# Performance work log

Hardware: AMD Instinct MI355X
Metric: run time of the kernel (lower is better)

Reference implementation:

```python
import jax, jax.numpy as jnp
import numpy as np

B, T, D, H = 2, 2048, 1024, 16
HD = D // H  # head_dim = 64

def setup_inputs() -> dict:
    key = jax.random.key(0)
    ks = jax.random.split(key, 5)
    s = 0.02
    return {
        "x": jax.random.normal(ks[0], (B, T, D), dtype=jnp.float32),
        "w_qkv": jax.random.normal(ks[1], (3 * D, D), dtype=jnp.float32) * s,
        "b_qkv": jax.random.normal(ks[2], (3 * D,), dtype=jnp.float32) * s,
        "w_proj": jax.random.normal(ks[3], (D, D), dtype=jnp.float32) * s,
        "b_proj": jax.random.normal(ks[4], (D,), dtype=jnp.float32) * s,
    }

def reference(x, w_qkv, b_qkv, w_proj, b_proj):
    b, t, c = x.shape
    h, hd = H, HD
    scale = hd ** -0.5
    # qkv projection (torch Linear: x @ W^T + b)
    qkv = x @ w_qkv.T + b_qkv                      # [b, t, 3c]
    q, k, v = jnp.split(qkv, 3, axis=-1)
    # b t (h d) -> b h t d
    reshape = lambda z: z.reshape(b, t, h, hd).transpose(0, 2, 1, 3)
    q, k, v = reshape(q), reshape(k), reshape(v)
    scores = jnp.einsum("bhqd,bhkd->bhqk", q, k) * scale  # [b, h, t, t]
    causal = jnp.triu(jnp.ones((t, t), dtype=bool), k=1)   # True above diag
    scores = jnp.where(causal[None, None], -jnp.inf, scores)
    attn = jax.nn.softmax(scores, axis=-1)
    out = jnp.einsum("bhqk,bhkd->bhqd", attn, v)            # [b, h, t, d]
    out = out.transpose(0, 2, 1, 3).reshape(b, t, c)        # b h t d -> b t (h d)
    return out @ w_proj.T + b_proj
```

## Files before the change

kernel.cpp:

```cpp
#include <hip/hip_runtime.h>
#include <hip/hip_bf16.h>

#define Bq 2
#define Tq 2048
#define Dq 1024
#define Hq 16
#define HDq 64

typedef __attribute__((ext_vector_type(8))) short short8;
typedef __attribute__((ext_vector_type(4))) float f32x4;

__device__ __forceinline__ unsigned short f2bf(float f) {
  union { float f; unsigned int i; } v; v.f = f;
  unsigned int r = v.i + 0x7fffu + ((v.i >> 16) & 1u);
  return (unsigned short)(r >> 16);
}
__device__ __forceinline__ unsigned short f2bf_fast(float f) {
  union { float f; unsigned int i; } v; v.f = f;
  return (unsigned short)((v.i + 0x8000u) >> 16);
}

__device__ __forceinline__ short8 cvt8(const float* __restrict__ g) {
  const float4* gp = (const float4*)g;
  float4 x0 = gp[0], x1 = gp[1];
  short8 v;
  v[0] = (short)f2bf(x0.x); v[1] = (short)f2bf(x0.y);
  v[2] = (short)f2bf(x0.z); v[3] = (short)f2bf(x0.w);
  v[4] = (short)f2bf(x1.x); v[5] = (short)f2bf(x1.y);
  v[6] = (short)f2bf(x1.z); v[7] = (short)f2bf(x1.w);
  return v;
}

__device__ __forceinline__ void async_cp16(const void* g, void* l) {
  __builtin_amdgcn_global_load_lds(
      (const __attribute__((address_space(1))) void*)g,
      (__attribute__((address_space(3))) void*)l, 16, 0, 0);
}

constexpr int NXC = (Bq * Tq * Dq) / 8;
constexpr int NW1C = (3 * Dq * Dq) / 8;
constexpr int NW2C = (Dq * Dq) / 8;

__global__ __launch_bounds__(256)
void cvt_all(const float* __restrict__ x, const float* __restrict__ w1,
             const float* __restrict__ w2, unsigned short* __restrict__ xo,
             unsigned short* __restrict__ w1o, unsigned short* __restrict__ w2o)
{
  int i = blockIdx.x * 256 + threadIdx.x;
  const float* src; unsigned short* dst; int j;
  if (i < NXC)              { src = x;  dst = xo;  j = i; }
  else if (i < NXC + NW1C)  { src = w1; dst = w1o; j = i - NXC; }
  else                      { src = w2; dst = w2o; j = i - NXC - NW1C; }
  *(short8*)&dst[(size_t)j * 8] = cvt8(src + (size_t)j * 8);
}

template<int EPI, int BM_, int BN_>
__global__ __launch_bounds__(256)
void gemm_bt(const unsigned short* __restrict__ Ab, const unsigned short* __restrict__ Wb,
             const float* __restrict__ bias, float* __restrict__ outp,
             int K, int N,
             unsigned short* __restrict__ qo, unsigned short* __restrict__ ko,
             unsigned short* __restrict__ vo)
{
  constexpr int WM = BM_ / 2, WN = BN_ / 2;
  constexpr int NI = WM / 16;
  constexpr int NJ = WN / 16;
  constexpr int NAI = BM_ / 32;
  constexpr int NBI = BN_ / 32;
  __shared__ unsigned short As[2 * BM_ * 32];
  __shared__ unsigned short Bs[2 * BN_ * 32];

  const int t = threadIdx.x;
  const int lane = t & 63, w = t >> 6;
  const int m0 = blockIdx.y * BM_, n0 = blockIdx.x * BN_;
  const int fr = lane & 15, qd = lane >> 4;
  const int wm = (w >> 1) * WM, wn = (w & 1) * WN;

  f32x4 acc[NI][NJ] = {};

  for (int k0 = 0; k0 < K; k0 += 64) {
    __syncthreads();
    #pragma unroll
    for (int j = 0; j < NAI; j++) {
      int G = j * 256 + t;
      int panel = G / (BM_ * 4), rowg = (G / 4) % BM_, colg = G & 3;
      async_cp16(Ab + (size_t)(m0 + rowg) * K + k0 + panel * 32 + colg * 8, &As[G * 8]);
    }
    #pragma unroll
    for (int j = 0; j < NBI; j++) {
      int G = j * 256 + t;
      int panel = G / (BN_ * 4), rowg = (G / 4) % BN_, colg = G & 3;
      async_cp16(Wb + (size_t)(n0 + rowg) * K + k0 + panel * 32 + colg * 8, &Bs[G * 8]);
    }
    __syncthreads();
    #pragma unroll
    for (int kh = 0; kh < 2; kh++) {
      short8 af[NI], bf[NJ];
      #pragma unroll
      for (int ib = 0; ib < NI; ib++)
        af[ib] = *(const short8*)&As[kh * (BM_ * 32) + (wm + ib * 16 + fr) * 32 + qd * 8];
      #pragma unroll
      for (int jb = 0; jb < NJ; jb++)
        bf[jb] = *(const short8*)&Bs[kh * (BN_ * 32) + (wn + jb * 16 + fr) * 32 + qd * 8];
      #pragma unroll
      for (int ib = 0; ib < NI; ib++)
        #pragma unroll
        for (int jb = 0; jb < NJ; jb++)
          acc[ib][jb] = __builtin_amdgcn_mfma_f32_16x16x32_bf16(af[ib], bf[jb], acc[ib][jb], 0, 0, 0);
    }
  }

  #pragma unroll
  for (int jb = 0; jb < NJ; jb++) {
    int col = n0 + wn + jb * 16 + fr;
    float bv = bias[col];
    if (EPI == 0) {
      int which = col >> 10;
      int rem = col & 1023;
      int hh = rem >> 6, dd = rem & 63;
      #pragma unroll
      for (int ib = 0; ib < NI; ib++) {
        int row4 = m0 + wm + ib * 16 + qd * 4;
        int bb = row4 >> 11, tt = row4 & (Tq - 1);
        if (which == 2) {
          unsigned lo = (unsigned)f2bf(acc[ib][jb][0] + bv)
                      | ((unsigned)f2bf(acc[ib][jb][1] + bv) << 16);
          unsigned hi = (unsigned)f2bf(acc[ib][jb][2] + bv)
                      | ((unsigned)f2bf(acc[ib][jb][3] + bv) << 16);
          uint2 pk; pk.x = lo; pk.y = hi;
          *(uint2*)&vo[((size_t)(bb * Hq + hh) * HDq + dd) * Tq + tt] = pk;
        } else {
          unsigned short* dst = (which == 0) ? qo : ko;
          #pragma unroll
          for (int r = 0; r < 4; r++)
            dst[((size_t)(bb * Hq + hh) * Tq + tt + r) * HDq + dd] = f2bf(acc[ib][jb][r] + bv);
        }
      }
    } else {
      #pragma unroll
      for (int ib = 0; ib < NI; ib++)
        #pragma unroll
        for (int r = 0; r < 4; r++) {
          int row = m0 + wm + ib * 16 + qd * 4 + r;
          outp[(size_t)row * N + col] = acc[ib][jb][r] + bv;
        }
    }
  }
}

constexpr int AP = 72;

template<bool DIAG>
__device__ __forceinline__ void strip_one(
    const short8 aq0, const short8 aq1,
    const short8 (&bk)[4][2], const short8 (&bv)[4][2], const short8 ones,
    unsigned short* __restrict__ PsRow, int fr, int qd, int qbase,
    f32x4 (&oacc)[4], f32x4& lacc, float SCL)
{
  f32x4 s4[4] = {};
  #pragma unroll
  for (int nb = 0; nb < 4; nb++) {
    s4[nb] = __builtin_amdgcn_mfma_f32_16x16x32_bf16(aq0, bk[nb][0], s4[nb], 0, 0, 0);
    s4[nb] = __builtin_amdgcn_mfma_f32_16x16x32_bf16(aq1, bk[nb][1], s4[nb], 0, 0, 0);
  }
  #pragma unroll
  for (int nb = 0; nb < 4; nb++)
    #pragma unroll
    for (int reg = 0; reg < 4; reg++) {
      float pv = exp2f(s4[nb][reg] * SCL);
      if (DIAG && (nb * 16 + fr) > (qbase + reg)) pv = 0.f;
      PsRow[(qd * 4 + reg) * AP + nb * 16 + fr] = f2bf_fast(pv);
    }
  short8 ap0 = *(const short8*)&PsRow[fr * AP + qd * 8];
  short8 ap1 = *(const short8*)&PsRow[fr * AP + 32 + qd * 8];
  lacc = __builtin_amdgcn_mfma_f32_16x16x32_bf16(ap0, ones, lacc, 0, 0, 0);
  lacc = __builtin_amdgcn_mfma_f32_16x16x32_bf16(ap1, ones, lacc, 0, 0, 0);
  #pragma unroll
  for (int db = 0; db < 4; db++) {
    oacc[db] = __builtin_amdgcn_mfma_f32_16x16x32_bf16(ap0, bv[db][0], oacc[db], 0, 0, 0);
    oacc[db] = __builtin_amdgcn_mfma_f32_16x16x32_bf16(ap1, bv[db][1], oacc[db], 0, 0, 0);
  }
}

template<bool SMALLDIAG>
__device__ __forceinline__ void strip_dual(
    const short8 (&aqB)[2], const short8 (&aqA)[2],
    const short8 (&bk)[4][2], const short8 (&bv)[4][2], const short8 ones,
    unsigned short* __restrict__ PsB, unsigned short* __restrict__ PsA,
    int fr, int qd, int qbase,
    f32x4 (&oB)[4], f32x4& lB, f32x4 (&oA)[4], f32x4& lA, float SCL)
{
  f32x4 sB[4] = {}, sA[4] = {};
  #pragma unroll
  for (int nb = 0; nb < 4; nb++) {
    sB[nb] = __builtin_amdgcn_mfma_f32_16x16x32_bf16(aqB[0], bk[nb][0], sB[nb], 0, 0, 0);
    sA[nb] = __builtin_amdgcn_mfma_f32_16x16x32_bf16(aqA[0], bk[nb][0], sA[nb], 0, 0, 0);
  }
  #pragma unroll
  for (int nb = 0; nb < 4; nb++) {
    sB[nb] = __builtin_amdgcn_mfma_f32_16x16x32_bf16(aqB[1], bk[nb][1], sB[nb], 0, 0, 0);
    sA[nb] = __builtin_amdgcn_mfma_f32_16x16x32_bf16(aqA[1], bk[nb][1], sA[nb], 0, 0, 0);
  }
  #pragma unroll
  for (int nb = 0; nb < 4; nb++)
    #pragma unroll
    for (int reg = 0; reg < 4; reg++) {
      float pvB = exp2f(sB[nb][reg] * SCL);
      float pvA = exp2f(sA[nb][reg] * SCL);
      if (SMALLDIAG && (nb * 16 + fr) > (qbase + reg)) pvA = 0.f;
      PsB[(qd * 4 + reg) * AP + nb * 16 + fr] = f2bf_fast(pvB);
      PsA[(qd * 4 + reg) * AP + nb * 16 + fr] = f2bf_fast(pvA);
    }
  short8 apB0 = *(const short8*)&PsB[fr * AP + qd * 8];
  short8 apB1 = *(const short8*)&PsB[fr * AP + 32 + qd * 8];
  short8 apA0 = *(const short8*)&PsA[fr * AP + qd * 8];
  short8 apA1 = *(const short8*)&PsA[fr * AP + 32 + qd * 8];
  lB = __builtin_amdgcn_mfma_f32_16x16x32_bf16(apB0, ones, lB, 0, 0, 0);
  lA = __builtin_amdgcn_mfma_f32_16x16x32_bf16(apA0, ones, lA, 0, 0, 0);
  lB = __builtin_amdgcn_mfma_f32_16x16x32_bf16(apB1, ones, lB, 0, 0, 0);
  lA = __builtin_amdgcn_mfma_f32_16x16x32_bf16(apA1, ones, lA, 0, 0, 0);
  #pragma unroll
  for (int db = 0; db < 4; db++) {
    oB[db] = __builtin_amdgcn_mfma_f32_16x16x32_bf16(apB0, bv[db][0], oB[db], 0, 0, 0);
    oA[db] = __builtin_amdgcn_mfma_f32_16x16x32_bf16(apA0, bv[db][0], oA[db], 0, 0, 0);
  }
  #pragma unroll
  for (int db = 0; db < 4; db++) {
    oB[db] = __builtin_amdgcn_mfma_f32_16x16x32_bf16(apB1, bv[db][1], oB[db], 0, 0, 0);
    oA[db] = __builtin_amdgcn_mfma_f32_16x16x32_bf16(apA1, bv[db][1], oA[db], 0, 0, 0);
  }
}

__global__ __launch_bounds__(256, 2)
void attn_fwd(const unsigned short* __restrict__ qb, const unsigned short* __restrict__ kb,
              const unsigned short* __restrict__ vtb, unsigned short* __restrict__ ab)
{
  __shared__ unsigned short Ks[2][64 * 64];
  __shared__ unsigned short Vts[2][64 * 64];
  __shared__ unsigned short Ps[128 * AP];

  const int t = threadIdx.x, w = t >> 6, lane = t & 63;
  const int fr = lane & 15, qd = lane >> 4;
  const int p = blockIdx.x;
  const int bh = blockIdx.y;
  const int sB = 31 - p;
  const int sA = p;
  const int s0t[2] = { sB * 64, sA * 64 };
  const int ktB = sB;
  const int qbase = w * 16 + qd * 4;

  short8 aq[2][2];
  #pragma unroll
  for (int tl = 0; tl < 2; tl++) {
    const unsigned short* Qg = qb + ((size_t)bh * Tq + s0t[tl]) * HDq;
    #pragma unroll
    for (int c = 0; c < 2; c++)
      aq[tl][c] = *(const short8*)(Qg + (w * 16 + fr) * 64 + c * 32 + qd * 8);
  }

  const unsigned short* Kbh = kb + (size_t)bh * Tq * HDq;
  const unsigned short* Vbh = vtb + (size_t)bh * HDq * Tq;

  const int off0 = ((qd ^ (fr & 7)) * 8);
  const int off1 = off0 ^ 32;

  const int G0 = 2 * w * 64 + lane, G1 = G0 + 64;
  const int r0 = G0 >> 3, g0 = (G0 & 7) ^ (r0 & 7);
  const int r1 = G1 >> 3, g1 = (G1 & 7) ^ (r1 & 7);

  short8 ones;
  #pragma unroll
  for (int j = 0; j < 8; j++) ones[j] = (short)0x3F80;

  f32x4 oacc[2][4] = {};
  f32x4 lacc[2] = {};
  const float SCL = 0.125f * 1.44269504088896f;

  unsigned short* PsB = &Ps[(0 * 64 + w * 16) * AP];
  unsigned short* PsA = &Ps[(1 * 64 + w * 16) * AP];

  async_cp16(Kbh + (size_t)r0 * 64 + g0 * 8, &Ks[0][G0 * 8]);
  async_cp16(Vbh + (size_t)r0 * Tq + g0 * 8, &Vts[0][G0 * 8]);
  async_cp16(Kbh + (size_t)r1 * 64 + g1 * 8, &Ks[0][G1 * 8]);
  async_cp16(Vbh + (size_t)r1 * Tq + g1 * 8, &Vts[0][G1 * 8]);

  for (int kt = 0; kt <= ktB; kt++) {
    const int cur = kt & 1;
    __syncthreads();
    if (kt < ktB) {
      const int nxt = cur ^ 1;
      const size_t kofs = (size_t)(kt + 1) * 64;
      async_cp16(Kbh + (kofs + r0) * 64 + g0 * 8, &Ks[nxt][G0 * 8]);
      async_cp16(Vbh + (size_t)r0 * Tq + kofs + g0 * 8, &Vts[nxt][G0 * 8]);
      async_cp16(Kbh + (kofs + r1) * 64 + g1 * 8, &Ks[nxt][G1 * 8]);
      async_cp16(Vbh + (size_t)r1 * Tq + kofs + g1 * 8, &Vts[nxt][G1 * 8]);
    }

    short8 bk[4][2], bv[4][2];
    #pragma unroll
    for (int nb = 0; nb < 4; nb++) {
      bk[nb][0] = *(const short8*)&Ks[cur][(nb * 16 + fr) * 64 + off0];
      bk[nb][1] = *(const short8*)&Ks[cur][(nb * 16 + fr) * 64 + off1];
      bv[nb][0] = *(const short8*)&Vts[cur][(nb * 16 + fr) * 64 + off0];
      bv[nb][1] = *(const short8*)&Vts[cur][(nb * 16 + fr) * 64 + off1];
    }

    if (kt < sA) {
      strip_dual<false>(aq[0], aq[1], bk, bv, ones, PsB, PsA, fr, qd, qbase,
                        oacc[0], lacc[0], oacc[1], lacc[1], SCL);
    } else if (kt == sA) {
      strip_dual<true >(aq[0], aq[1], bk, bv, ones, PsB, PsA, fr, qd, qbase,
                        oacc[0], lacc[0], oacc[1], lacc[1], SCL);
    } else if (kt == ktB) {
      strip_one<true >(aq[0][0], aq[0][1], bk, bv, ones, PsB, fr, qd, qbase,
                       oacc[0], lacc[0], SCL);
    } else {
      strip_one<false>(aq[0][0], aq[0][1], bk, bv, ones, PsB, fr, qd, qbase,
                       oacc[0], lacc[0], SCL);
    }
  }

  #pragma unroll
  for (int tl = 0; tl < 2; tl++)
    #pragma unroll
    for (int reg = 0; reg < 4; reg++) {
      float linv = 1.0f / lacc[tl][reg];
      size_t rowoff = ((size_t)(bh >> 4) * Tq + s0t[tl] + w * 16 + qd * 4 + reg) * Dq
                    + (bh & 15) * HDq;
      #pragma unroll
      for (int db = 0; db < 4; db++)
        ab[rowoff + db * 16 + fr] = f2bf(oacc[tl][db][reg] * linv);
    }
}

extern "C" void kernel_launch(void* const* d_in, const int* in_sizes, int n_in,
                              void* d_out, int out_size, void* d_ws, size_t ws_size,
                              hipStream_t stream) {
  const float* x      = (const float*)d_in[0];
  const float* w_qkv  = (const float*)d_in[1];
  const float* b_qkv  = (const float*)d_in[2];
  const float* w_proj = (const float*)d_in[3];
  const float* b_proj = (const float*)d_in[4];
  float* out = (float*)d_out;

  unsigned short* ws = (unsigned short*)d_ws;
  const size_t NE = (size_t)Bq * Hq * Tq * HDq;
  unsigned short* qb  = ws;
  unsigned short* kb  = ws + NE;
  unsigned short* vtb = ws + 2 * NE;
  unsigned short* ab  = ws + 3 * NE;
  unsigned short* xb  = ws + 4 * NE;
  unsigned short* wqb = xb + (size_t)NXC * 8;
  unsigned short* wpb = wqb + (size_t)NW1C * 8;

  dim3 blk(256);
  cvt_all<<<dim3((NXC + NW1C + NW2C) >> 8), blk, 0, stream>>>(x, w_qkv, w_proj, xb, wqb, wpb);

  dim3 g1(3 * Dq / 128, Bq * Tq / 128);
  gemm_bt<0, 128, 128><<<g1, blk, 0, stream>>>(xb, wqb, b_qkv, nullptr,
                                               Dq, 3 * Dq, qb, kb, vtb);
  dim3 g2(16, Bq * Hq);
  attn_fwd<<<g2, blk, 0, stream>>>(qb, kb, vtb, ab);
  dim3 g3(Dq / 128, Bq * Tq / 64);
  gemm_bt<1, 64, 128><<<g3, blk, 0, stream>>>(ab, wpb, b_proj, out,
                                              Dq, Dq, nullptr, nullptr, nullptr);
}
```

Baseline: 190.9 us.

## Compute transposed scores in attention, reshuffle P in registers, drop LDS P buffer

The attention kernel now computes S^T (K as the A operand), so each lane holds probabilities along the key dimension. It packs them with v_cvt_pk_bf16_f32 and rearranges them with permlane swaps into the PV operand layout, which removes the LDS round trip for P. The softmax scale times log2(e) is folded into Q in the QKV GEMM epilogue. The paired causal-balancing tiles are replaced by one q-tile per block with 4 blocks/SM occupancy and setprio around the MFMA bursts. The cost is losing the load-balanced strip pairing, plus gfx950-specific permlane instructions and a different rounding of P.

```diff
diff --git a/kernel.cpp b/kernel.cpp
--- a/kernel.cpp
+++ b/kernel.cpp
@@ -14,10 +14,6 @@
   union { float f; unsigned int i; } v; v.f = f;
   unsigned int r = v.i + 0x7fffu + ((v.i >> 16) & 1u);
   return (unsigned short)(r >> 16);
-}
-__device__ __forceinline__ unsigned short f2bf_fast(float f) {
-  union { float f; unsigned int i; } v; v.f = f;
-  return (unsigned short)((v.i + 0x8000u) >> 16);
 }
 
 __device__ __forceinline__ short8 cvt8(const float* __restrict__ g) {
@@ -37,9 +33,16 @@
       (__attribute__((address_space(3))) void*)l, 16, 0, 0);
 }
 
+__device__ __forceinline__ void permswap(unsigned &a, unsigned &b) {
+  asm("v_permlane32_swap_b32 %0, %1" : "+v"(a), "+v"(b));
+  asm("v_permlane16_swap_b32 %0, %1" : "+v"(a), "+v"(b));
+}
+
 constexpr int NXC = (Bq * Tq * Dq) / 8;
 constexpr int NW1C = (3 * Dq * Dq) / 8;
 constexpr int NW2C = (Dq * Dq) / 8;
+
+#define QSCL 0.18033688011112042f
 
 __global__ __launch_bounds__(256)
 void cvt_all(const float* __restrict__ x, const float* __restrict__ w1,
@@ -131,9 +134,11 @@
           *(uint2*)&vo[((size_t)(bb * Hq + hh) * HDq + dd) * Tq + tt] = pk;
         } else {
           unsigned short* dst = (which == 0) ? qo : ko;
+          float scl = (which == 0) ? QSCL : 1.0f;
           #pragma unroll
           for (int r = 0; r < 4; r++)
-            dst[((size_t)(bb * Hq + hh) * Tq + tt + r) * HDq + dd] = f2bf(acc[ib][jb][r] + bv);
+            dst[((size_t)(bb * Hq + hh) * Tq + tt + r) * HDq + dd] =
+                f2bf((acc[ib][jb][r] + bv) * scl);
         }
       }
     } else {
@@ -148,31 +153,62 @@
   }
 }
 
-constexpr int AP = 72;
 
 template<bool DIAG>
-__device__ __forceinline__ void strip_one(
-    const short8 aq0, const short8 aq1,
-    const short8 (&bk)[4][2], const short8 (&bv)[4][2], const short8 ones,
-    unsigned short* __restrict__ PsRow, int fr, int qd, int qbase,
-    f32x4 (&oacc)[4], f32x4& lacc, float SCL)
+__device__ __forceinline__ void strip_iter(
+    const unsigned short* __restrict__ Ksb, const unsigned short* __restrict__ Vtsb,
+    const short8 (&aq)[2], const short8 ones,
+    int fr, int qd, int off0, int off1, int thr,
+    f32x4 (&oacc)[4], f32x4& lacc)
 {
+  short8 bk[4][2];
+  #pragma unroll
+  for (int nb = 0; nb < 4; nb++) {
+    bk[nb][0] = *(const short8*)&Ksb[(nb * 16 + fr) * 64 + off0];
+    bk[nb][1] = *(const short8*)&Ksb[(nb * 16 + fr) * 64 + off1];
+  }
   f32x4 s4[4] = {};
+  __builtin_amdgcn_s_setprio(1);
+  #pragma unroll
+  for (int nb = 0; nb < 4; nb++)
+    s4[nb] = __builtin_amdgcn_mfma_f32_16x16x32_bf16(bk[nb][0], aq[0], s4[nb], 0, 0, 0);
+  #pragma unroll
+  for (int nb = 0; nb < 4; nb++)
+    s4[nb] = __builtin_amdgcn_mfma_f32_16x16x32_bf16(bk[nb][1], aq[1], s4[nb], 0, 0, 0);
+  __builtin_amdgcn_s_setprio(0);
+
+  unsigned x[4][2];
   #pragma unroll
   for (int nb = 0; nb < 4; nb++) {
-    s4[nb] = __builtin_amdgcn_mfma_f32_16x16x32_bf16(aq0, bk[nb][0], s4[nb], 0, 0, 0);
-    s4[nb] = __builtin_amdgcn_mfma_f32_16x16x32_bf16(aq1, bk[nb][1], s4[nb], 0, 0, 0);
-  }
-  #pragma unroll
-  for (int nb = 0; nb < 4; nb++)
+    float p[4];
     #pragma unroll
     for (int reg = 0; reg < 4; reg++) {
-      float pv = exp2f(s4[nb][reg] * SCL);
-      if (DIAG && (nb * 16 + fr) > (qbase + reg)) pv = 0.f;
-      PsRow[(qd * 4 + reg) * AP + nb * 16 + fr] = f2bf_fast(pv);
-    }
-  short8 ap0 = *(const short8*)&PsRow[fr * AP + qd * 8];
-  short8 ap1 = *(const short8*)&PsRow[fr * AP + 32 + qd * 8];
+      p[reg] = exp2f(s4[nb][reg]);
+      if (DIAG && (nb * 16 + qd * 4 + reg) > thr) p[reg] = 0.f;
+    }
+    asm("v_cvt_pk_bf16_f32 %0, %1, %2" : "=v"(x[nb][0]) : "v"(p[0]), "v"(p[1]));
+    asm("v_cvt_pk_bf16_f32 %0, %1, %2" : "=v"(x[nb][1]) : "v"(p[2]), "v"(p[3]));
+  }
+  permswap(x[0][0], x[1][0]);
+  permswap(x[0][1], x[1][1]);
+  permswap(x[2][0], x[3][0]);
+  permswap(x[2][1], x[3][1]);
+
+  short8 ap0, ap1;
+  {
+    union { unsigned u[4]; short8 s; } c0, c1;
+    c0.u[0] = x[0][0]; c0.u[1] = x[0][1]; c0.u[2] = x[1][0]; c0.u[3] = x[1][1];
+    c1.u[0] = x[2][0]; c1.u[1] = x[2][1]; c1.u[2] = x[3][0]; c1.u[3] = x[3][1];
+    ap0 = c0.s; ap1 = c1.s;
+  }
+
+  short8 bv[4][2];
+  #pragma unroll
+  for (int db = 0; db < 4; db++) {
+    bv[db][0] = *(const short8*)&Vtsb[(db * 16 + fr) * 64 + off0];
+    bv[db][1] = *(const short8*)&Vtsb[(db * 16 + fr) * 64 + off1];
+  }
+  __builtin_amdgcn_s_setprio(1);
   lacc = __builtin_amdgcn_mfma_f32_16x16x32_bf16(ap0, ones, lacc, 0, 0, 0);
   lacc = __builtin_amdgcn_mfma_f32_16x16x32_bf16(ap1, ones, lacc, 0, 0, 0);
   #pragma unroll
@@ -180,83 +216,28 @@
     oacc[db] = __builtin_amdgcn_mfma_f32_16x16x32_bf16(ap0, bv[db][0], oacc[db], 0, 0, 0);
     oacc[db] = __builtin_amdgcn_mfma_f32_16x16x32_bf16(ap1, bv[db][1], oacc[db], 0, 0, 0);
   }
-}
-
-template<bool SMALLDIAG>
-__device__ __forceinline__ void strip_dual(
-    const short8 (&aqB)[2], const short8 (&aqA)[2],
-    const short8 (&bk)[4][2], const short8 (&bv)[4][2], const short8 ones,
-    unsigned short* __restrict__ PsB, unsigned short* __restrict__ PsA,
-    int fr, int qd, int qbase,
-    f32x4 (&oB)[4], f32x4& lB, f32x4 (&oA)[4], f32x4& lA, float SCL)
-{
-  f32x4 sB[4] = {}, sA[4] = {};
-  #pragma unroll
-  for (int nb = 0; nb < 4; nb++) {
-    sB[nb] = __builtin_amdgcn_mfma_f32_16x16x32_bf16(aqB[0], bk[nb][0], sB[nb], 0, 0, 0);
-    sA[nb] = __builtin_amdgcn_mfma_f32_16x16x32_bf16(aqA[0], bk[nb][0], sA[nb], 0, 0, 0);
-  }
-  #pragma unroll
-  for (int nb = 0; nb < 4; nb++) {
-    sB[nb] = __builtin_amdgcn_mfma_f32_16x16x32_bf16(aqB[1], bk[nb][1], sB[nb], 0, 0, 0);
-    sA[nb] = __builtin_amdgcn_mfma_f32_16x16x32_bf16(aqA[1], bk[nb][1], sA[nb], 0, 0, 0);
-  }
-  #pragma unroll
-  for (int nb = 0; nb < 4; nb++)
-    #pragma unroll
-    for (int reg = 0; reg < 4; reg++) {
-      float pvB = exp2f(sB[nb][reg] * SCL);
-      float pvA = exp2f(sA[nb][reg] * SCL);
-      if (SMALLDIAG && (nb * 16 + fr) > (qbase + reg)) pvA = 0.f;
-      PsB[(qd * 4 + reg) * AP + nb * 16 + fr] = f2bf_fast(pvB);
-      PsA[(qd * 4 + reg) * AP + nb * 16 + fr] = f2bf_fast(pvA);
-    }
-  short8 apB0 = *(const short8*)&PsB[fr * AP + qd * 8];
-  short8 apB1 = *(const short8*)&PsB[fr * AP + 32 + qd * 8];
-  short8 apA0 = *(const short8*)&PsA[fr * AP + qd * 8];
-  short8 apA1 = *(const short8*)&PsA[fr * AP + 32 + qd * 8];
-  lB = __builtin_amdgcn_mfma_f32_16x16x32_bf16(apB0, ones, lB, 0, 0, 0);
-  lA = __builtin_amdgcn_mfma_f32_16x16x32_bf16(apA0, ones, lA, 0, 0, 0);
-  lB = __builtin_amdgcn_mfma_f32_16x16x32_bf16(apB1, ones, lB, 0, 0, 0);
-  lA = __builtin_amdgcn_mfma_f32_16x16x32_bf16(apA1, ones, lA, 0, 0, 0);
-  #pragma unroll
-  for (int db = 0; db < 4; db++) {
-    oB[db] = __builtin_amdgcn_mfma_f32_16x16x32_bf16(apB0, bv[db][0], oB[db], 0, 0, 0);
-    oA[db] = __builtin_amdgcn_mfma_f32_16x16x32_bf16(apA0, bv[db][0], oA[db], 0, 0, 0);
-  }
-  #pragma unroll
-  for (int db = 0; db < 4; db++) {
-    oB[db] = __builtin_amdgcn_mfma_f32_16x16x32_bf16(apB1, bv[db][1], oB[db], 0, 0, 0);
-    oA[db] = __builtin_amdgcn_mfma_f32_16x16x32_bf16(apA1, bv[db][1], oA[db], 0, 0, 0);
-  }
-}
-
-__global__ __launch_bounds__(256, 2)
+  __builtin_amdgcn_s_setprio(0);
+}
+
+__global__ __launch_bounds__(256, 4)
 void attn_fwd(const unsigned short* __restrict__ qb, const unsigned short* __restrict__ kb,
               const unsigned short* __restrict__ vtb, unsigned short* __restrict__ ab)
 {
   __shared__ unsigned short Ks[2][64 * 64];
   __shared__ unsigned short Vts[2][64 * 64];
-  __shared__ unsigned short Ps[128 * AP];
 
   const int t = threadIdx.x, w = t >> 6, lane = t & 63;
   const int fr = lane & 15, qd = lane >> 4;
-  const int p = blockIdx.x;
-  const int bh = blockIdx.y;
-  const int sB = 31 - p;
-  const int sA = p;
-  const int s0t[2] = { sB * 64, sA * 64 };
-  const int ktB = sB;
-  const int qbase = w * 16 + qd * 4;
-
-  short8 aq[2][2];
-  #pragma unroll
-  for (int tl = 0; tl < 2; tl++) {
-    const unsigned short* Qg = qb + ((size_t)bh * Tq + s0t[tl]) * HDq;
-    #pragma unroll
-    for (int c = 0; c < 2; c++)
-      aq[tl][c] = *(const short8*)(Qg + (w * 16 + fr) * 64 + c * 32 + qd * 8);
-  }
+  const int bh = blockIdx.x;
+  const int s = 31 - (int)blockIdx.y;
+  const int s0 = s * 64;
+  const int thr = w * 16 + fr;
+
+  short8 aq[2];
+  const unsigned short* Qg = qb + ((size_t)bh * Tq + s0) * HDq;
+  #pragma unroll
+  for (int c = 0; c < 2; c++)
+    aq[c] = *(const short8*)(Qg + (w * 16 + fr) * 64 + c * 32 + qd * 8);
 
   const unsigned short* Kbh = kb + (size_t)bh * Tq * HDq;
   const unsigned short* Vbh = vtb + (size_t)bh * HDq * Tq;
@@ -272,65 +253,36 @@
   #pragma unroll
   for (int j = 0; j < 8; j++) ones[j] = (short)0x3F80;
 
-  f32x4 oacc[2][4] = {};
-  f32x4 lacc[2] = {};
-  const float SCL = 0.125f * 1.44269504088896f;
-
-  unsigned short* PsB = &Ps[(0 * 64 + w * 16) * AP];
-  unsigned short* PsA = &Ps[(1 * 64 + w * 16) * AP];
+  f32x4 oacc[4] = {};
+  f32x4 lacc = {};
 
   async_cp16(Kbh + (size_t)r0 * 64 + g0 * 8, &Ks[0][G0 * 8]);
   async_cp16(Vbh + (size_t)r0 * Tq + g0 * 8, &Vts[0][G0 * 8]);
   async_cp16(Kbh + (size_t)r1 * 64 + g1 * 8, &Ks[0][G1 * 8]);
   async_cp16(Vbh + (size_t)r1 * Tq + g1 * 8, &Vts[0][G1 * 8]);
 
-  for (int kt = 0; kt <= ktB; kt++) {
-    const int cur = kt & 1;
+  for (int kt = 0; kt < s; kt++) {
+    const int cur = kt & 1, nxt = cur ^ 1;
     __syncthreads();
-    if (kt < ktB) {
-      const int nxt = cur ^ 1;
-      const size_t kofs = (size_t)(kt + 1) * 64;
-      async_cp16(Kbh + (kofs + r0) * 64 + g0 * 8, &Ks[nxt][G0 * 8]);
-      async_cp16(Vbh + (size_t)r0 * Tq + kofs + g0 * 8, &Vts[nxt][G0 * 8]);
-      async_cp16(Kbh + (kofs + r1) * 64 + g1 * 8, &Ks[nxt][G1 * 8]);
-      async_cp16(Vbh + (size_t)r1 * Tq + kofs + g1 * 8, &Vts[nxt][G1 * 8]);
-    }
-
-    short8 bk[4][2], bv[4][2];
-    #pragma unroll
-    for (int nb = 0; nb < 4; nb++) {
-      bk[nb][0] = *(const short8*)&Ks[cur][(nb * 16 + fr) * 64 + off0];
-      bk[nb][1] = *(const short8*)&Ks[cur][(nb * 16 + fr) * 64 + off1];
-      bv[nb][0] = *(const short8*)&Vts[cur][(nb * 16 + fr) * 64 + off0];
-      bv[nb][1] = *(const short8*)&Vts[cur][(nb * 16 + fr) * 64 + off1];
-    }
-
-    if (kt < sA) {
-      strip_dual<false>(aq[0], aq[1], bk, bv, ones, PsB, PsA, fr, qd, qbase,
-                        oacc[0], lacc[0], oacc[1], lacc[1], SCL);
-    } else if (kt == sA) {
-      strip_dual<true >(aq[0], aq[1], bk, bv, ones, PsB, PsA, fr, qd, qbase,
-                        oacc[0], lacc[0], oacc[1], lacc[1], SCL);
-    } else if (kt == ktB) {
-      strip_one<true >(aq[0][0], aq[0][1], bk, bv, ones, PsB, fr, qd, qbase,
-                       oacc[0], lacc[0], SCL);
-    } else {
-      strip_one<false>(aq[0][0], aq[0][1], bk, bv, ones, PsB, fr, qd, qbase,
-                       oacc[0], lacc[0], SCL);
-    }
-  }
-
-  #pragma unroll
-  for (int tl = 0; tl < 2; tl++)
-    #pragma unroll
-    for (int reg = 0; reg < 4; reg++) {
-      float linv = 1.0f / lacc[tl][reg];
-      size_t rowoff = ((size_t)(bh >> 4) * Tq + s0t[tl] + w * 16 + qd * 4 + reg) * Dq
-                    + (bh & 15) * HDq;
-      #pragma unroll
-      for (int db = 0; db < 4; db++)
-        ab[rowoff + db * 16 + fr] = f2bf(oacc[tl][db][reg] * linv);
-    }
+    const size_t kofs = (size_t)(kt + 1) * 64;
+    async_cp16(Kbh + (kofs + r0) * 64 + g0 * 8, &Ks[nxt][G0 * 8]);
+    async_cp16(Vbh + (size_t)r0 * Tq + kofs + g0 * 8, &Vts[nxt][G0 * 8]);
+    async_cp16(Kbh + (kofs + r1) * 64 + g1 * 8, &Ks[nxt][G1 * 8]);
+    async_cp16(Vbh + (size_t)r1 * Tq + kofs + g1 * 8, &Vts[nxt][G1 * 8]);
+    strip_iter<false>(Ks[cur], Vts[cur], aq, ones, fr, qd, off0, off1, thr, oacc, lacc);
+  }
+  __syncthreads();
+  strip_iter<true>(Ks[s & 1], Vts[s & 1], aq, ones, fr, qd, off0, off1, thr, oacc, lacc);
+
+  #pragma unroll
+  for (int reg = 0; reg < 4; reg++) {
+    float linv = 1.0f / lacc[reg];
+    size_t rowoff = ((size_t)(bh >> 4) * Tq + s0 + w * 16 + qd * 4 + reg) * Dq
+                  + (bh & 15) * HDq;
+    #pragma unroll
+    for (int db = 0; db < 4; db++)
+      ab[rowoff + db * 16 + fr] = f2bf(oacc[db][reg] * linv);
+  }
 }
 
 extern "C" void kernel_launch(void* const* d_in, const int* in_sizes, int n_in,
@@ -359,7 +311,7 @@
   dim3 g1(3 * Dq / 128, Bq * Tq / 128);
   gemm_bt<0, 128, 128><<<g1, blk, 0, stream>>>(xb, wqb, b_qkv, nullptr,
                                                Dq, 3 * Dq, qb, kb, vtb);
-  dim3 g2(16, Bq * Hq);
+  dim3 g2(Bq * Hq, Tq / 64);
   attn_fwd<<<g2, blk, 0, stream>>>(qb, kb, vtb, ab);
   dim3 g3(Dq / 128, Bq * Tq / 64);
   gemm_bt<1, 64, 128><<<g3, blk, 0, stream>>>(ab, wpb, b_proj, out,
```

Result: faster. 175.0 us (-8.3%).
